# Performance work log

Hardware: AMD Instinct MI355X
Metric: run time of the kernel (lower is better)

Reference implementation:

```python
import jax, jax.numpy as jnp
import numpy as np

B, D, L = 16384, 1024, 4


def setup_inputs() -> dict:
    key = jax.random.key(0)
    ks = jax.random.split(key, 5)
    scale = 1.0 / np.sqrt(D)
    x = jax.random.normal(ks[0], (B, D), dtype=jnp.float32)
    # torch nn.Linear default init: U(-1/sqrt(fan_in), 1/sqrt(fan_in))
    Ws = jax.random.uniform(ks[1], (L, D, D), jnp.float32, -scale, scale)
    bs = jax.random.uniform(ks[2], (L, D), jnp.float32, -scale, scale)
    Wo = jax.random.uniform(ks[3], (D, D), jnp.float32, -scale, scale)
    bo = jax.random.uniform(ks[4], (D,), jnp.float32, -scale, scale)
    return {"x": x, "Ws": Ws, "bs": bs, "Wo": Wo, "bo": bo}


def reference(x, Ws, bs, Wo, bo):
    # torch: matmul(x[:, :, None], x[:, None, :]).sum(2) == x * x.sum(-1, keepdims=True)
    interactions = jax.nn.relu(x * jnp.sum(x, axis=-1, keepdims=True))  # (B, D)
    h = x
    for i in range(L):  # fixed small layer count
        h = jax.nn.relu(h @ Ws[i].T + bs[i])  # torch Linear: y = x W^T + b
    out = ((h + interactions) * 0.5) @ Wo.T + bo
    return out
```

## Files before the change

### kernel.cpp

```cpp
#include <hip/hip_runtime.h>


#define DDIM 1024
#define BROWS 16384

typedef __attribute__((ext_vector_type(8))) short s8v;
typedef __attribute__((ext_vector_type(4))) float f4v;

__device__ __forceinline__ unsigned short f2bf(float f) {
    unsigned int u = __float_as_uint(f);
    u += 0x7fffu + ((u >> 16) & 1u);
    return (unsigned short)(u >> 16);
}
__device__ __forceinline__ float bf2f(unsigned short u) {
    return __uint_as_float(((unsigned int)u) << 16);
}
__device__ __forceinline__ void gld16(const void* g, void* l) {
    __builtin_amdgcn_global_load_lds(
        (const __attribute__((address_space(1))) unsigned int*)g,
        (__attribute__((address_space(3))) unsigned int*)l, 16, 0, 0);
}

__global__ __launch_bounds__(256) void prep_kernel(
    const float* __restrict__ x, unsigned short* __restrict__ xb,
    float* __restrict__ rowsum)
{
    const int row = blockIdx.x;
    const int t = threadIdx.x;
    const float4 v = *(const float4*)(x + (size_t)row * DDIM + t * 4);
    ushort4 o;
    o.x = f2bf(v.x); o.y = f2bf(v.y); o.z = f2bf(v.z); o.w = f2bf(v.w);
    *(ushort4*)(xb + (size_t)row * DDIM + t * 4) = o;
    float s = v.x + v.y + v.z + v.w;
    #pragma unroll
    for (int off = 32; off > 0; off >>= 1) s += __shfl_down(s, off, 64);
    __shared__ float red[4];
    const int wave = t >> 6, lane = t & 63;
    if (lane == 0) red[wave] = s;
    __syncthreads();
    if (t == 0) rowsum[row] = red[0] + red[1] + red[2] + red[3];
}

__global__ __launch_bounds__(256) void cvt_kernel(
    const float* __restrict__ Ws, const float* __restrict__ Wo,
    unsigned short* __restrict__ out)
{
    const int i = (blockIdx.x * 256 + threadIdx.x) * 4;
    const float* src = (i < 4 * DDIM * DDIM) ? (Ws + i) : (Wo + (i - 4 * DDIM * DDIM));
    const float4 v = *(const float4*)src;
    ushort4 o;
    o.x = f2bf(v.x); o.y = f2bf(v.y); o.z = f2bf(v.z); o.w = f2bf(v.w);
    *(ushort4*)(out + i) = o;
}

template <int MODE>
__global__ __launch_bounds__(256, 2) void gemm_bt(
    const unsigned short* __restrict__ A,
    const unsigned short* __restrict__ Bw,
    const float* __restrict__ bias,
    void* __restrict__ out,
    const unsigned short* __restrict__ xb,
    const float* __restrict__ rowsum)
{
    constexpr int K = DDIM, N = DDIM;
    __shared__ unsigned short smem[4][128 * 32];

    const int t = threadIdx.x;
    const int wave = t >> 6, lane = t & 63;
    const int wm = wave & 1, wn = wave >> 1;
    const int rowBase = blockIdx.x * 128;
    const int colBase = blockIdx.y * 128;

    f4v acc[4][4] = {};

    const int c0r = t >> 2, c0k = (t & 3) * 8;
    const int mrow = lane & 15;
    const int koff = (lane >> 4) * 8;

    for (int kt = 0; kt < K; kt += 64) {
        if (kt) __syncthreads();
        const unsigned short* a0 = A  + (size_t)(rowBase + c0r) * K + kt + c0k;
        const unsigned short* b0 = Bw + (size_t)(colBase + c0r) * K + kt + c0k;
        gld16(a0,               (char*)smem[0] + t * 16);
        gld16(a0 + 64 * K,      (char*)smem[0] + (t + 256) * 16);
        gld16(b0,               (char*)smem[2] + t * 16);
        gld16(b0 + 64 * K,      (char*)smem[2] + (t + 256) * 16);
        gld16(a0 + 32,          (char*)smem[1] + t * 16);
        gld16(a0 + 64 * K + 32, (char*)smem[1] + (t + 256) * 16);
        gld16(b0 + 32,          (char*)smem[3] + t * 16);
        gld16(b0 + 64 * K + 32, (char*)smem[3] + (t + 256) * 16);
        __syncthreads();

        #pragma unroll
        for (int s = 0; s < 2; ++s) {
            s8v af[4], bfr[4];
            #pragma unroll
            for (int mi = 0; mi < 4; ++mi)
                af[mi] = *(const s8v*)&smem[s][(wm * 64 + mi * 16 + mrow) * 32 + koff];
            #pragma unroll
            for (int ni = 0; ni < 4; ++ni)
                bfr[ni] = *(const s8v*)&smem[2 + s][(wn * 64 + ni * 16 + mrow) * 32 + koff];
            #pragma unroll
            for (int mi = 0; mi < 4; ++mi)
                #pragma unroll
                for (int ni = 0; ni < 4; ++ni)
                    acc[mi][ni] = __builtin_amdgcn_mfma_f32_16x16x32_bf16(
                        af[mi], bfr[ni], acc[mi][ni], 0, 0, 0);
        }
    }

    const int quad = lane >> 4;
    if (MODE == 2) {
        float* o = (float*)out;
        #pragma unroll
        for (int ni = 0; ni < 4; ++ni) {
            const int n = colBase + wn * 64 + ni * 16 + mrow;
            const float bv = bias[n];
            #pragma unroll
            for (int mi = 0; mi < 4; ++mi)
                #pragma unroll
                for (int r = 0; r < 4; ++r) {
                    const int row = rowBase + wm * 64 + mi * 16 + quad * 4 + r;
                    o[(size_t)row * N + n] = acc[mi][ni][r] + bv;
                }
        }
    } else {
        __syncthreads();
        unsigned short* sC = (unsigned short*)smem;
        #pragma unroll
        for (int ni = 0; ni < 4; ++ni) {
            const int n = wn * 64 + ni * 16 + mrow;
            const float bv = bias[colBase + n];
            #pragma unroll
            for (int mi = 0; mi < 4; ++mi)
                #pragma unroll
                for (int r = 0; r < 4; ++r) {
                    const int row = wm * 64 + mi * 16 + quad * 4 + r;
                    float v = acc[mi][ni][r] + bv;
                    v = v > 0.f ? v : 0.f;
                    sC[row * 128 + n] = f2bf(v);
                }
        }
        __syncthreads();
        unsigned short* o16 = (unsigned short*)out;
        #pragma unroll
        for (int i = 0; i < 8; ++i) {
            const int idx = t + i * 256;
            const int row = idx >> 4, ch = idx & 15;
            s8v c = *(const s8v*)&sC[row * 128 + ch * 8];
            if (MODE == 1) {
                const float rsv = rowsum[rowBase + row];
                const s8v xv = *(const s8v*)&xb[(size_t)(rowBase + row) * DDIM + colBase + ch * 8];
                #pragma unroll
                for (int j = 0; j < 8; ++j) {
                    float it = bf2f((unsigned short)xv[j]) * rsv;
                    it = it > 0.f ? it : 0.f;
                    const float v = 0.5f * (bf2f((unsigned short)c[j]) + it);
                    c[j] = (short)f2bf(v);
                }
            }
            *(s8v*)&o16[(size_t)(rowBase + row) * DDIM + colBase + ch * 8] = c;
        }
    }
}

extern "C" void kernel_launch(void* const* d_in, const int* in_sizes, int n_in,
                              void* d_out, int out_size, void* d_ws, size_t ws_size,
                              hipStream_t stream) {
    const float* x  = (const float*)d_in[0];
    const float* Ws = (const float*)d_in[1];
    const float* bs = (const float*)d_in[2];
    const float* Wo = (const float*)d_in[3];
    const float* bo = (const float*)d_in[4];
    float* out = (float*)d_out;

    char* ws = (char*)d_ws;
    unsigned short* xb  = (unsigned short*)(ws);
    unsigned short* h0  = (unsigned short*)(ws + 33554432);
    unsigned short* h1  = (unsigned short*)(ws + 67108864);
    unsigned short* wb  = (unsigned short*)(ws + 100663296);
    float*          rsm = (float*)(ws + 111149056);

    prep_kernel<<<BROWS, 256, 0, stream>>>(x, xb, rsm);
    cvt_kernel<<<(5 * DDIM * DDIM) / 1024, 256, 0, stream>>>(Ws, Wo, wb);

    const size_t WSZ = (size_t)DDIM * DDIM;
    dim3 g(BROWS / 128, DDIM / 128);
    gemm_bt<0><<<g, 256, 0, stream>>>(xb, wb,           bs,            h0, nullptr, nullptr);
    gemm_bt<0><<<g, 256, 0, stream>>>(h0, wb + 1 * WSZ, bs + 1 * DDIM, h1, nullptr, nullptr);
    gemm_bt<0><<<g, 256, 0, stream>>>(h1, wb + 2 * WSZ, bs + 2 * DDIM, h0, nullptr, nullptr);
    gemm_bt<1><<<g, 256, 0, stream>>>(h0, wb + 3 * WSZ, bs + 3 * DDIM, h1, xb, rsm);
    gemm_bt<2><<<g, 256, 0, stream>>>(h1, wb + 4 * WSZ, bo,            out, nullptr, nullptr);
}
```

Before: 373.4 us.

## Fuse prep and weight conversion kernels, stage fp32 output through LDS, raise occupancy

Merges the input prep and weight conversion into one launch so both run in a single grid. The final fp32 GEMM epilogue now writes through shared memory in two halves so global stores are coalesced float4 rows instead of strided scalar stores. Launch bounds go from 2 to 3 blocks per CU, which may force register spills given the 64-float accumulator per thread.

```diff
diff --git a/kernel.cpp b/kernel.cpp
--- a/kernel.cpp
+++ b/kernel.cpp
@@ -21,40 +21,42 @@
         (__attribute__((address_space(3))) unsigned int*)l, 16, 0, 0);
 }
 
-__global__ __launch_bounds__(256) void prep_kernel(
-    const float* __restrict__ x, unsigned short* __restrict__ xb,
-    float* __restrict__ rowsum)
+__global__ __launch_bounds__(256) void prep_cvt_kernel(
+    const float* __restrict__ x,  const float* __restrict__ Ws,
+    const float* __restrict__ Wo, unsigned short* __restrict__ xb,
+    unsigned short* __restrict__ wb, float* __restrict__ rowsum)
 {
-    const int row = blockIdx.x;
     const int t = threadIdx.x;
-    const float4 v = *(const float4*)(x + (size_t)row * DDIM + t * 4);
-    ushort4 o;
-    o.x = f2bf(v.x); o.y = f2bf(v.y); o.z = f2bf(v.z); o.w = f2bf(v.w);
-    *(ushort4*)(xb + (size_t)row * DDIM + t * 4) = o;
-    float s = v.x + v.y + v.z + v.w;
-    #pragma unroll
-    for (int off = 32; off > 0; off >>= 1) s += __shfl_down(s, off, 64);
-    __shared__ float red[4];
-    const int wave = t >> 6, lane = t & 63;
-    if (lane == 0) red[wave] = s;
-    __syncthreads();
-    if (t == 0) rowsum[row] = red[0] + red[1] + red[2] + red[3];
-}
-
-__global__ __launch_bounds__(256) void cvt_kernel(
-    const float* __restrict__ Ws, const float* __restrict__ Wo,
-    unsigned short* __restrict__ out)
-{
-    const int i = (blockIdx.x * 256 + threadIdx.x) * 4;
-    const float* src = (i < 4 * DDIM * DDIM) ? (Ws + i) : (Wo + (i - 4 * DDIM * DDIM));
-    const float4 v = *(const float4*)src;
-    ushort4 o;
-    o.x = f2bf(v.x); o.y = f2bf(v.y); o.z = f2bf(v.z); o.w = f2bf(v.w);
-    *(ushort4*)(out + i) = o;
+    if (blockIdx.x < BROWS) {
+        const int row = blockIdx.x;
+        const float4 v = *(const float4*)(x + (size_t)row * DDIM + t * 4);
+        ushort4 o;
+        o.x = f2bf(v.x); o.y = f2bf(v.y); o.z = f2bf(v.z); o.w = f2bf(v.w);
+        *(ushort4*)(xb + (size_t)row * DDIM + t * 4) = o;
+        float s = v.x + v.y + v.z + v.w;
+        #pragma unroll
+        for (int off = 32; off > 0; off >>= 1) s += __shfl_down(s, off, 64);
+        __shared__ float red[4];
+        const int wave = t >> 6, lane = t & 63;
+        if (lane == 0) red[wave] = s;
+        __syncthreads();
+        if (t == 0) rowsum[row] = red[0] + red[1] + red[2] + red[3];
+    } else {
+        const int base = (blockIdx.x - BROWS) * 1024;
+        #pragma unroll
+        for (int j = 0; j < 4; ++j) {
+            const int idx = base + j * 256 + t;
+            const float4 v = (idx < 4 * 262144) ? ((const float4*)Ws)[idx]
+                                                : ((const float4*)Wo)[idx - 4 * 262144];
+            ushort4 o;
+            o.x = f2bf(v.x); o.y = f2bf(v.y); o.z = f2bf(v.z); o.w = f2bf(v.w);
+            ((ushort4*)wb)[idx] = o;
+        }
+    }
 }
 
 template <int MODE>
-__global__ __launch_bounds__(256, 2) void gemm_bt(
+__global__ __launch_bounds__(256, 3) void gemm_bt(
     const unsigned short* __restrict__ A,
     const unsigned short* __restrict__ Bw,
     const float* __restrict__ bias,
@@ -72,10 +74,10 @@
     const int colBase = blockIdx.y * 128;
 
     f4v acc[4][4] = {};
-
     const int c0r = t >> 2, c0k = (t & 3) * 8;
     const int mrow = lane & 15;
-    const int koff = (lane >> 4) * 8;
+    const int quad = lane >> 4;
+    const int koff = quad * 8;
 
     for (int kt = 0; kt < K; kt += 64) {
         if (kt) __syncthreads();
@@ -90,7 +92,6 @@
         gld16(b0 + 32,          (char*)smem[3] + t * 16);
         gld16(b0 + 64 * K + 32, (char*)smem[3] + (t + 256) * 16);
         __syncthreads();
-
         #pragma unroll
         for (int s = 0; s < 2; ++s) {
             s8v af[4], bfr[4];
@@ -109,20 +110,32 @@
         }
     }
 
-    const int quad = lane >> 4;
     if (MODE == 2) {
+        float* sCf = (float*)smem;
         float* o = (float*)out;
-        #pragma unroll
-        for (int ni = 0; ni < 4; ++ni) {
-            const int n = colBase + wn * 64 + ni * 16 + mrow;
-            const float bv = bias[n];
-            #pragma unroll
-            for (int mi = 0; mi < 4; ++mi)
-                #pragma unroll
-                for (int r = 0; r < 4; ++r) {
-                    const int row = rowBase + wm * 64 + mi * 16 + quad * 4 + r;
-                    o[(size_t)row * N + n] = acc[mi][ni][r] + bv;
+        #pragma unroll 1
+        for (int half = 0; half < 2; ++half) {
+            __syncthreads();
+            if (wm == half) {
+                #pragma unroll
+                for (int ni = 0; ni < 4; ++ni) {
+                    const int n = wn * 64 + ni * 16 + mrow;
+                    const float bv = bias[colBase + n];
+                    #pragma unroll
+                    for (int mi = 0; mi < 4; ++mi)
+                        #pragma unroll
+                        for (int r = 0; r < 4; ++r)
+                            sCf[(mi * 16 + quad * 4 + r) * 128 + n] = acc[mi][ni][r] + bv;
                 }
+            }
+            __syncthreads();
+            #pragma unroll
+            for (int i = 0; i < 8; ++i) {
+                const int idx = t + i * 256;
+                const int row = idx >> 5, ch = idx & 31;
+                const float4 v = ((const float4*)sCf)[idx];
+                ((float4*)(o + (size_t)(rowBase + half * 64 + row) * N + colBase))[ch] = v;
+            }
         }
     } else {
         __syncthreads();
@@ -155,8 +168,7 @@
                 for (int j = 0; j < 8; ++j) {
                     float it = bf2f((unsigned short)xv[j]) * rsv;
                     it = it > 0.f ? it : 0.f;
-                    const float v = 0.5f * (bf2f((unsigned short)c[j]) + it);
-                    c[j] = (short)f2bf(v);
+                    c[j] = (short)f2bf(0.5f * (bf2f((unsigned short)c[j]) + it));
                 }
             }
             *(s8v*)&o16[(size_t)(rowBase + row) * DDIM + colBase + ch * 8] = c;
@@ -181,8 +193,7 @@
     unsigned short* wb  = (unsigned short*)(ws + 100663296);
     float*          rsm = (float*)(ws + 111149056);
 
-    prep_kernel<<<BROWS, 256, 0, stream>>>(x, xb, rsm);
-    cvt_kernel<<<(5 * DDIM * DDIM) / 1024, 256, 0, stream>>>(Ws, Wo, wb);
+    prep_cvt_kernel<<<BROWS + 1280, 256, 0, stream>>>(x, Ws, Wo, xb, wb, rsm);
 
     const size_t WSZ = (size_t)DDIM * DDIM;
     dim3 g(BROWS / 128, DDIM / 128);
```

Result: no change. 367.0 us (-1.7%).
